# Performance work log

Measured on AMD Instinct MI355X. Metric: run time of the kernel, lower is better.

The kernel has to match this reference:

```python
import jax, jax.numpy as jnp
import numpy as np

D_MODEL = 1024
D_STATE = 64
D_CONV = 4
EXPAND = 2
N_HEADS = 16
HEAD_DIM = 64
ATTN_EVERY = 6
N_LAYERS = 6
D_INNER = D_MODEL * EXPAND
N_SSM = sum(1 for i in range(N_LAYERS) if i % ATTN_EVERY != ATTN_EVERY - 1)
CHUNK = 128  # time-chunk for checkpointed scan


def layer_norm(x, g, b, eps=1e-5):
    mu = jnp.mean(x, axis=-1, keepdims=True)
    var = jnp.mean((x - mu) ** 2, axis=-1, keepdims=True)
    return (x - mu) * jax.lax.rsqrt(var + eps) * g + b


def ssm_layer(x, Wi, cw, cb, Wo, g, b):
    # x: [B, T, d_model]
    Bsz, T, _ = x.shape
    proj = x @ Wi  # [B, T, d_inner + 2*d_state]
    xs = proj[..., :D_INNER]
    Bm = proj[..., D_INNER:D_INNER + D_STATE]
    Cm = proj[..., D_INNER + D_STATE:]
    # causal depthwise conv1d (pad left d_conv-1 == torch pad-both then slice [:T])
    xc = jax.lax.conv_general_dilated(
        xs.transpose(0, 2, 1), cw[:, None, :], (1,), [(D_CONV - 1, 0)],
        feature_group_count=D_INNER, dimension_numbers=('NCH', 'OIH', 'NCH'))
    xc = jax.nn.silu(xc + cb[None, :, None]).transpose(0, 2, 1)  # [B, T, d_inner]
    A = -jnp.exp(jnp.full((D_INNER,), np.float32(np.log(0.5)), x.dtype))  # = -0.5
    nC = T // CHUNK
    u = xc.transpose(1, 0, 2).reshape(nC, CHUNK, Bsz, D_INNER)
    bm = Bm.transpose(1, 0, 2).reshape(nC, CHUNK, Bsz, D_STATE)
    cm = Cm.transpose(1, 0, 2).reshape(nC, CHUNK, Bsz, D_STATE)

    def step(h, inp):
        u_t, b_t, c_t = inp  # [B,d_inner], [B,d_state], [B,d_state]
        h = A[None, :, None] * h + u_t[:, :, None] * b_t[:, None, :]
        y = jnp.einsum('bds,bs->bd', h, c_t)
        return h, y

    @jax.checkpoint
    def chunk_fn(h, ch):
        return jax.lax.scan(step, h, ch)

    h0 = jnp.zeros((Bsz, D_INNER, D_STATE), x.dtype)
    _, y = jax.lax.scan(chunk_fn, h0, (u, bm, cm))  # [nC, CHUNK, B, d_inner]
    y = y.reshape(T, Bsz, D_INNER).transpose(1, 0, 2)
    return layer_norm(y @ Wo + x, g, b)


def attn_layer(x, wq, wk, wv, wo, g, b):
    Bsz, T, _ = x.shape
    sh = (Bsz, T, N_HEADS, HEAD_DIM)
    q = (x @ wq).reshape(sh)
    k = (x @ wk).reshape(sh)
    v = (x @ wv).reshape(sh)
    scores = jnp.einsum('bqhd,bkhd->bhqk', q, k) * (HEAD_DIM ** -0.5)
    mask = jnp.tril(jnp.ones((T, T), bool))
    scores = jnp.where(mask[None, None], scores, -jnp.inf)
    w = jax.nn.softmax(scores, axis=-1)
    o = jnp.einsum('bhqk,bkhd->bqhd', w, v).reshape(Bsz, T, N_HEADS * HEAD_DIM)
    return layer_norm(o @ wo + x, g, b)


def setup_inputs() -> dict:
    key = jax.random.key(0)
    ks = jax.random.split(key, 8)
    s = jnp.float32(0.02)
    d_attn = N_HEADS * HEAD_DIM
    return {
        'x': jax.random.normal(ks[0], (2, 2048, D_MODEL), jnp.float32),
        'in_proj_w': jax.random.normal(ks[1], (N_SSM, D_MODEL, D_INNER + 2 * D_STATE), jnp.float32) * s,
        'conv_w': jax.random.normal(ks[2], (N_SSM, D_INNER, D_CONV), jnp.float32) * s,
        'conv_b': jnp.zeros((N_SSM, D_INNER), jnp.float32),
        'out_proj_w': jax.random.normal(ks[3], (N_SSM, D_INNER, D_MODEL), jnp.float32) * s,
        'ssm_ln_g': jnp.ones((N_SSM, D_MODEL), jnp.float32),
        'ssm_ln_b': jnp.zeros((N_SSM, D_MODEL), jnp.float32),
        'wq': jax.random.normal(ks[4], (D_MODEL, d_attn), jnp.float32) * s,
        'wk': jax.random.normal(ks[5], (D_MODEL, d_attn), jnp.float32) * s,
        'wv': jax.random.normal(ks[6], (D_MODEL, d_attn), jnp.float32) * s,
        'wo': jax.random.normal(ks[7], (d_attn, D_MODEL), jnp.float32) * s,
        'attn_ln_g': jnp.ones((D_MODEL,), jnp.float32),
        'attn_ln_b': jnp.zeros((D_MODEL,), jnp.float32),
    }


def reference(x, in_proj_w, conv_w, conv_b, out_proj_w, ssm_ln_g, ssm_ln_b,
              wq, wk, wv, wo, attn_ln_g, attn_ln_b):
    ssm_idx = 0
    for i in range(N_LAYERS):
        if i % ATTN_EVERY == ATTN_EVERY - 1:
            x = attn_layer(x, wq, wk, wv, wo, attn_ln_g, attn_ln_b)
        else:
            j = ssm_idx
            x = ssm_layer(x, in_proj_w[j], conv_w[j], conv_b[j], out_proj_w[j],
                          ssm_ln_g[j], ssm_ln_b[j])
            ssm_idx += 1
    return x
```

## Files before the change

### kernel.cpp

```cpp
#include <hip/hip_runtime.h>

typedef __attribute__((ext_vector_type(4))) float v4f;
typedef __attribute__((ext_vector_type(4))) float f32x4;
typedef __attribute__((ext_vector_type(8))) __bf16 bf16x8;
typedef __attribute__((ext_vector_type(4))) unsigned short v4u16;

__device__ __forceinline__ unsigned short f2bf(float f) {
    union { float f; unsigned u; } v; v.f = f;
    unsigned r = v.u + 0x7fffu + ((v.u >> 16) & 1u);
    return (unsigned short)(r >> 16);
}
__device__ __forceinline__ float bf2f(unsigned short s) {
    union { unsigned u; float f; } v; v.u = ((unsigned)s) << 16;
    return v.f;
}

#define GLDS16(gp, lp) __builtin_amdgcn_global_load_lds( \
    (const __attribute__((address_space(1))) void*)(gp), \
    (__attribute__((address_space(3))) void*)(lp), 16, 0, 0)

template <int MODE>
__global__ __launch_bounds__(256) void gemm_bf16(
    const unsigned short* __restrict__ A,
    const unsigned short* __restrict__ Bt,
    void* __restrict__ Cout,
    int M, int N, int K, int ldk)
{
    __shared__ __align__(16) unsigned short lA[4096];
    __shared__ __align__(16) unsigned short lB[4096];
    const int tid  = threadIdx.x;
    const int wave = tid >> 6;
    const int lane = tid & 63;
    const int wr = wave >> 1, wc = wave & 1;
    const long m0 = (long)blockIdx.x * 128, n0 = (long)blockIdx.y * 128;
    const int kz = blockIdx.z;
    const long koff = (long)kz * K;

    const int srow = tid >> 2;
    const int scol = (tid & 3) * 8;
    const unsigned short* gA0 = A  + (m0 + srow) * (long)ldk + koff + scol;
    const unsigned short* gB0 = Bt + (n0 + srow) * (long)ldk + koff + scol;
    const long rstride = 64l * ldk;
    unsigned short* lA0 = lA + wave * 512;
    unsigned short* lB0 = lB + wave * 512;

    const int fr = lane & 15;
    const int kg = (lane >> 4) * 8;
    const int arow = (wr * 64 + fr) * 32 + kg;
    const int brow = (wc * 64 + fr) * 32 + kg;

    f32x4 acc[4][4] = {};

    for (int k0 = 0; k0 < K; k0 += 32) {
        __syncthreads();
        GLDS16(gA0 + k0,           lA0);
        GLDS16(gA0 + k0 + rstride, lA0 + 2048);
        GLDS16(gB0 + k0,           lB0);
        GLDS16(gB0 + k0 + rstride, lB0 + 2048);
        __syncthreads();
        bf16x8 af[4], bb[4];
#pragma unroll
        for (int m = 0; m < 4; ++m)
            af[m] = *(const bf16x8*)(lA + arow + m * 512);
#pragma unroll
        for (int n = 0; n < 4; ++n)
            bb[n] = *(const bf16x8*)(lB + brow + n * 512);
#pragma unroll
        for (int m = 0; m < 4; ++m)
#pragma unroll
            for (int n = 0; n < 4; ++n)
                acc[m][n] = __builtin_amdgcn_mfma_f32_16x16x32_bf16(
                    af[m], bb[n], acc[m][n], 0, 0, 0);
    }

    const int lgrp = lane >> 4;
    if constexpr (MODE == 0) {
        float* C = (float*)Cout + (long)kz * M * (long)N;
        float* Cbase = C + (m0 + wr * 64 + lgrp * 4) * (long)N
                         + n0 + wc * 64 + fr;
#pragma unroll
        for (int m = 0; m < 4; ++m)
#pragma unroll
            for (int n = 0; n < 4; ++n) {
                float* cp = Cbase + m * 16 * (long)N + n * 16;
#pragma unroll
                for (int r = 0; r < 4; ++r)
                    cp[r * (long)N] = acc[m][n][r];
            }
    } else if constexpr (MODE == 1) {
        unsigned short* C = (unsigned short*)Cout;
        unsigned short* Cbase = C + (m0 + wr * 64 + lgrp * 4) * (long)N
                                  + n0 + wc * 64 + fr;
#pragma unroll
        for (int m = 0; m < 4; ++m)
#pragma unroll
            for (int n = 0; n < 4; ++n) {
                unsigned short* cp = Cbase + m * 16 * (long)N + n * 16;
#pragma unroll
                for (int r = 0; r < 4; ++r)
                    cp[r * (long)N] = f2bf(acc[m][n][r]);
            }
    } else {
        unsigned short* C = (unsigned short*)Cout;
#pragma unroll
        for (int n = 0; n < 4; ++n) {
            int col = (int)n0 + wc * 64 + n * 16 + fr;
            int hb = col >> 6;
            int s = hb >> 4, h = hb & 15;
            int d = (n & 3) * 16 + fr;
            float sc = (s == 0) ? 0.125f * 1.44269504f : 1.f;
            long obase = ((long)(s * 32) + h) * 2048 * 64 + d;
#pragma unroll
            for (int m = 0; m < 4; ++m) {
#pragma unroll
                for (int r = 0; r < 4; ++r) {
                    int row = (int)m0 + wr * 64 + lgrp * 4 + m * 16 + r;
                    int b = row >> 11, t = row & 2047;
                    C[obase + ((long)b * 16 * 2048 + t) * 64] =
                        f2bf(acc[m][n][r] * sc);
                }
            }
        }
    }
}

__global__ __launch_bounds__(256) void transW(
    const float* __restrict__ in, unsigned short* __restrict__ outp,
    int K, int N, long inl, long outl)
{
    __shared__ unsigned short tile[64][65];
    const float* ip = in + (long)blockIdx.z * inl;
    unsigned short* op = outp + (long)blockIdx.z * outl;
    int n0 = blockIdx.x * 64, k0 = blockIdx.y * 64;
    int cc = threadIdx.x & 63, rr = threadIdx.x >> 6;
#pragma unroll
    for (int i = 0; i < 16; ++i) {
        int r = i * 4 + rr;
        tile[r][cc] = f2bf(ip[(long)(k0 + r) * N + n0 + cc]);
    }
    __syncthreads();
#pragma unroll
    for (int i = 0; i < 16; ++i) {
        int r = i * 4 + rr;
        op[(long)(n0 + r) * K + k0 + cc] = tile[cc][r];
    }
}

__global__ __launch_bounds__(256) void transV(
    const unsigned short* __restrict__ qkvb, unsigned short* __restrict__ vtb)
{
    __shared__ unsigned short tile[64][72];
    const int tid = threadIdx.x;
    const int bh = blockIdx.x, t0 = blockIdx.y * 64;
    const unsigned short* vg = qkvb + 64l * 2048 * 64
                              + (long)bh * 2048 * 64 + (long)t0 * 64;
    const int row = tid >> 2, c0 = (tid & 3) * 16;
#pragma unroll
    for (int i = 0; i < 4; ++i)
        *(v4u16*)(&tile[row][c0 + i * 4]) =
            *(const v4u16*)(vg + row * 64 + c0 + i * 4);
    __syncthreads();
    const int d = tid >> 2, tc = (tid & 3) * 16;
    unsigned short* vo = vtb + (long)bh * 64 * 2048 + (long)d * 2048 + t0 + tc;
#pragma unroll
    for (int i = 0; i < 4; ++i) {
        v4u16 w;
#pragma unroll
        for (int j = 0; j < 4; ++j) w[j] = tile[tc + i * 4 + j][d];
        *(v4u16*)(vo + i * 4) = w;
    }
}

__global__ __launch_bounds__(256) void init_x(
    const float* __restrict__ xin, float* __restrict__ x,
    unsigned short* __restrict__ xb)
{
    long i = ((long)blockIdx.x * 256 + threadIdx.x) * 4;
    v4f v = *(const v4f*)(xin + i);
    *(v4f*)(x + i) = v;
    v4u16 pk;
#pragma unroll
    for (int j = 0; j < 4; ++j) pk[j] = f2bf(v[j]);
    *(v4u16*)(xb + i) = pk;
}

__global__ __launch_bounds__(256) void conv_t(
    const unsigned short* __restrict__ projb,
    const float* __restrict__ cw,
    const float* __restrict__ cb,
    unsigned short* __restrict__ ut)
{
    __shared__ unsigned short tile[68][68];
    const int tid = threadIdx.x;
    const int r0 = blockIdx.x * 64, d0 = blockIdx.y * 64;

    for (int idx = tid; idx < 1072; idx += 256) {
        int row = idx >> 4, c4 = (idx & 15) * 4;
        int gr = r0 - 3 + row;
        v4u16 v;
        if (gr >= 0) v = *(const v4u16*)(projb + (long)gr * 2176 + d0 + c4);
        else         v = (v4u16){0, 0, 0, 0};
        *(v4u16*)(&tile[row][c4]) = v;
    }
    __syncthreads();

    const int lane = tid & 63;
    const int wave = tid >> 6;
    const int t = (r0 + lane) & 2047;
#pragma unroll
    for (int dd = 0; dd < 16; ++dd) {
        int d = wave * 16 + dd;
        int dch = d0 + d;
        v4f w = *(const v4f*)(cw + (long)dch * 4);
        float a = cb[dch];
#pragma unroll
        for (int kk = 0; kk < 4; ++kk) {
            float xv = (t - 3 + kk >= 0) ? bf2f(tile[lane + kk][d]) : 0.f;
            a += xv * w[kk];
        }
        float sv = a / (1.f + __expf(-a));
        ut[(long)dch * 4096 + r0 + lane] = f2bf(sv);
    }
}

__global__ __launch_bounds__(256) void band_ssm(
    const unsigned short* __restrict__ projb,
    const unsigned short* __restrict__ ut,
    unsigned short* __restrict__ yb)
{
    __shared__ __align__(16) unsigned short lU[16384];
    __shared__ __align__(16) unsigned short lB[4096];
    __shared__ __align__(16) unsigned short lC[2048];
    __shared__ __align__(16) unsigned short lP[2048];

    const int tid = threadIdx.x;
    const int wave = tid >> 6, lane = tid & 63;
    const int r0 = blockIdx.x * 32;
    const int d0 = blockIdx.y * 256;
    const int wb = r0 - 32;

#pragma unroll
    for (int p = 0; p < 8; ++p) {
        int chunk = p * 256 + tid;
        int dd = chunk >> 3, j = chunk & 7;
        int off = wb + j * 8; if (off < 0) off = 0;
        uint4 v = *(const uint4*)(ut + (long)(d0 + dd) * 4096 + off);
        *(uint4*)((char*)lU + ((dd * 128 + j * 16) ^ ((dd & 7) << 4))) = v;
    }
#pragma unroll
    for (int p = 0; p < 2; ++p) {
        int chunk = p * 256 + tid;
        int c = chunk >> 3, j = chunk & 7;
        int rc = wb + c; if (rc < 0) rc = 0;
        uint4 v = *(const uint4*)(projb + (long)rc * 2176 + 2048 + j * 8);
        *(uint4*)((char*)lB + ((c * 128 + j * 16) ^ ((c & 7) << 4))) = v;
    }
    {
        int i = tid >> 3, j = tid & 7;
        uint4 v = *(const uint4*)(projb + (long)(r0 + i) * 2176 + 2112 + j * 8);
        *(uint4*)((char*)lC + ((i * 128 + j * 16) ^ ((i & 7) << 4))) = v;
    }
    __syncthreads();

    const int lrow = lane & 15, lgrp = lane >> 4;
    const int sw = (lrow & 7) << 4;

    {
        f32x4 s[2] = {};
        int cb_ = wave * 16 + lrow;
        bf16x8 b0 = *(const bf16x8*)((const char*)lB + ((cb_ * 128 + lgrp * 16) ^ sw));
        bf16x8 b1 = *(const bf16x8*)((const char*)lB + ((cb_ * 128 + 64 + lgrp * 16) ^ sw));
#pragma unroll
        for (int ti = 0; ti < 2; ++ti) {
            int ar = ti * 16 + lrow;
            bf16x8 a0 = *(const bf16x8*)((const char*)lC + ((ar * 128 + lgrp * 16) ^ sw));
            bf16x8 a1 = *(const bf16x8*)((const char*)lC + ((ar * 128 + 64 + lgrp * 16) ^ sw));
            s[ti] = __builtin_amdgcn_mfma_f32_16x16x32_bf16(a0, b0, s[ti], 0, 0, 0);
            s[ti] = __builtin_amdgcn_mfma_f32_16x16x32_bf16(a1, b1, s[ti], 0, 0, 0);
        }
#pragma unroll
        for (int ti = 0; ti < 2; ++ti) {
#pragma unroll
            for (int r = 0; r < 4; ++r) {
                int i = ti * 16 + lgrp * 4 + r;
                int c = wave * 16 + lrow;
                int k = i + 32 - c;
                int t = (r0 + i) & 2047;
                float p = 0.f;
                if (k >= 0 && k <= 31 && k <= t) {
                    float f = exp2f(-(float)k);
                    p = s[ti][r] * ((k & 1) ? -f : f);
                }
                *(unsigned short*)((char*)lP + ((i * 128 + c * 2) ^ ((i & 7) << 4)))
                    = f2bf(p);
            }
        }
    }
    __syncthreads();

    {
        bf16x8 pa[2][2];
#pragma unroll
        for (int ti = 0; ti < 2; ++ti) {
            int pr = ti * 16 + lrow;
            pa[ti][0] = *(const bf16x8*)((const char*)lP + ((pr * 128 + lgrp * 16) ^ sw));
            pa[ti][1] = *(const bf16x8*)((const char*)lP + ((pr * 128 + 64 + lgrp * 16) ^ sw));
        }
#pragma unroll
        for (int dt = 0; dt < 4; ++dt) {
            int dd = wave * 64 + dt * 16 + lrow;
            bf16x8 u0 = *(const bf16x8*)((const char*)lU + ((dd * 128 + lgrp * 16) ^ sw));
            bf16x8 u1 = *(const bf16x8*)((const char*)lU + ((dd * 128 + 64 + lgrp * 16) ^ sw));
#pragma unroll
            for (int ti = 0; ti < 2; ++ti) {
                f32x4 acc = {};
                acc = __builtin_amdgcn_mfma_f32_16x16x32_bf16(pa[ti][0], u0, acc, 0, 0, 0);
                acc = __builtin_amdgcn_mfma_f32_16x16x32_bf16(pa[ti][1], u1, acc, 0, 0, 0);
#pragma unroll
                for (int r = 0; r < 4; ++r) {
                    int i = ti * 16 + lgrp * 4 + r;
                    yb[(long)(r0 + i) * 2048 + d0 + wave * 64 + dt * 16 + lrow]
                        = f2bf(acc[r]);
                }
            }
        }
    }
}

__global__ __launch_bounds__(256) void ln_fuse(
    const float* __restrict__ tmp0, const float* __restrict__ tmp1,
    const float* __restrict__ xres,
    const float* __restrict__ g, const float* __restrict__ b,
    float* __restrict__ xout, unsigned short* __restrict__ xbout)
{
    int row = blockIdx.x;
    int tid = threadIdx.x;
    v4f t0 = *(const v4f*)(tmp0 + (long)row * 1024 + tid * 4);
    v4f t1 = *(const v4f*)(tmp1 + (long)row * 1024 + tid * 4);
    v4f rv = *(const v4f*)(xres + (long)row * 1024 + tid * 4);
    v4f v = t0 + t1 + rv;
    float s = v[0] + v[1] + v[2] + v[3];
    float q = v[0]*v[0] + v[1]*v[1] + v[2]*v[2] + v[3]*v[3];
#pragma unroll
    for (int m = 32; m >= 1; m >>= 1) {
        s += __shfl_xor(s, m, 64);
        q += __shfl_xor(q, m, 64);
    }
    __shared__ float ls[4], lq[4];
    int wave = tid >> 6, lane = tid & 63;
    if (lane == 0) { ls[wave] = s; lq[wave] = q; }
    __syncthreads();
    s = ls[0] + ls[1] + ls[2] + ls[3];
    q = lq[0] + lq[1] + lq[2] + lq[3];
    float mean = s * (1.f / 1024.f);
    float var  = q * (1.f / 1024.f) - mean * mean;
    float rstd = rsqrtf(var + 1e-5f);
    v4f gv = *(const v4f*)(g + tid * 4);
    v4f bv = *(const v4f*)(b + tid * 4);
    v4f o;
#pragma unroll
    for (int i = 0; i < 4; ++i) o[i] = (v[i] - mean) * rstd * gv[i] + bv[i];
    *(v4f*)(xout + (long)row * 1024 + tid * 4) = o;
    v4u16 pk;
#pragma unroll
    for (int i = 0; i < 4; ++i) pk[i] = f2bf(o[i]);
    *(v4u16*)(xbout + (long)row * 1024 + tid * 4) = pk;
}

__global__ __launch_bounds__(256) void attn_mfma(
    const unsigned short* __restrict__ qkvb,
    const unsigned short* __restrict__ vtb,
    unsigned short* __restrict__ ob)
{
    __shared__ __align__(16) unsigned short lK[2][4096];
    __shared__ __align__(16) unsigned short lV[2][4096];
    __shared__ __align__(16) unsigned short lP[4][1024];

    const int tid  = threadIdx.x;
    const int wave = tid >> 6;
    const int lane = tid & 63;
    const int bh = blockIdx.x;
    const int qt = blockIdx.y;
    const long base = (long)bh * 2048 * 64;
    const unsigned short* Qg = qkvb + base;
    const char* Kc = (const char*)(qkvb + 32l * 2048 * 64 + base);
    const char* Vc = (const char*)(vtb + (long)bh * 64 * 2048);

    const int qr0  = qt * 64 + wave * 16;
    const int lrow = lane & 15;
    const int lgrp = lane >> 4;

    bf16x8 qf[2];
    {
        const unsigned short* qp = Qg + (long)(qr0 + lrow) * 64 + lgrp * 8;
        qf[0] = *(const bf16x8*)(qp);
        qf[1] = *(const bf16x8*)(qp + 32);
    }

    f32x4 oacc[4] = {};
    float l[4] = {0.f, 0.f, 0.f, 0.f};

    const int o0  = wave * 1024 + lane * 16;
    const int ta  = o0 >> 7;
    const int cba = (o0 & 127) ^ ((ta & 7) << 4);
    const int o1  = o0 + 4096;
    const int tb  = o1 >> 7;
    const int cbb = (o1 & 127) ^ ((tb & 7) << 4);
    const int ldst = wave * 1024;

#define STAGE(kb_, buf_) do { \
    const int t0_ = (kb_) * 64; \
    GLDS16(Kc + (long)(t0_ + ta) * 128 + cba, (char*)lK[buf_] + ldst); \
    GLDS16(Kc + (long)(t0_ + tb) * 128 + cbb, (char*)lK[buf_] + 4096 + ldst); \
    GLDS16(Vc + (long)ta * 4096 + t0_ * 2 + cba, (char*)lV[buf_] + ldst); \
    GLDS16(Vc + (long)tb * 4096 + t0_ * 2 + cbb, (char*)lV[buf_] + 4096 + ldst); \
} while (0)

    unsigned short* Pw = lP[wave];
    const int nkv = qt + 1;
    STAGE(0, 0);

    for (int kb = 0; kb < nkv; ++kb) {
        const int cur = kb & 1;
        const int t0 = kb * 64;
        __syncthreads();
        if (kb + 1 < nkv) STAGE(kb + 1, cur ^ 1);

        f32x4 sacc[4] = {};
#pragma unroll
        for (int f = 0; f < 4; ++f) {
            int t = f * 16 + lrow;
            int sw = (t & 7) << 4;
            int ob0 = t * 128 + lgrp * 16;
#pragma unroll
            for (int c = 0; c < 2; ++c) {
                bf16x8 kf = *(const bf16x8*)((const char*)lK[cur] + ((ob0 + c * 64) ^ sw));
                sacc[f] = __builtin_amdgcn_mfma_f32_16x16x32_bf16(
                    qf[c], kf, sacc[f], 0, 0, 0);
            }
        }

        float ps[4] = {0.f, 0.f, 0.f, 0.f};
#pragma unroll
        for (int f = 0; f < 4; ++f) {
            int tg = t0 + f * 16 + lrow;
            int t = f * 16 + lrow;
#pragma unroll
            for (int r = 0; r < 4; ++r) {
                int qg = qr0 + lgrp * 4 + r;
                float p = (tg <= qg) ? exp2f(sacc[f][r]) : 0.f;
                ps[r] += p;
                int row = lgrp * 4 + r;
                int po = (row * 128 + t * 2) ^ ((row & 7) << 4);
                *(unsigned short*)((char*)Pw + po) = f2bf(p);
            }
        }
#pragma unroll
        for (int msk = 1; msk < 16; msk <<= 1)
#pragma unroll
            for (int r = 0; r < 4; ++r)
                ps[r] += __shfl_xor(ps[r], msk, 64);
#pragma unroll
        for (int r = 0; r < 4; ++r) l[r] += ps[r];

#pragma unroll
        for (int tc = 0; tc < 2; ++tc) {
            int po = (lrow * 128 + tc * 64 + lgrp * 16) ^ ((lrow & 7) << 4);
            bf16x8 pf = *(const bf16x8*)((const char*)Pw + po);
#pragma unroll
            for (int fd = 0; fd < 4; ++fd) {
                int d = fd * 16 + lrow;
                int vo = (d * 128 + tc * 64 + lgrp * 16) ^ ((d & 7) << 4);
                bf16x8 vf = *(const bf16x8*)((const char*)lV[cur] + vo);
                oacc[fd] = __builtin_amdgcn_mfma_f32_16x16x32_bf16(
                    pf, vf, oacc[fd], 0, 0, 0);
            }
        }
    }
#undef STAGE

    const int b = bh >> 4, h = bh & 15;
#pragma unroll
    for (int r = 0; r < 4; ++r) {
        float inv = 1.f / l[r];
        int qg = qr0 + lgrp * 4 + r;
        unsigned short* orow = ob + ((long)b * 2048 + qg) * 1024 + h * 64;
#pragma unroll
        for (int fd = 0; fd < 4; ++fd)
            orow[fd * 16 + lrow] = f2bf(oacc[fd][r] * inv);
    }
}

extern "C" void kernel_launch(void* const* d_in, const int* in_sizes, int n_in,
                              void* d_out, int out_size, void* d_ws, size_t ws_size,
                              hipStream_t stream) {
    const float* x_in = (const float*)d_in[0];
    const float* Wi   = (const float*)d_in[1];
    const float* cw   = (const float*)d_in[2];
    const float* cb   = (const float*)d_in[3];
    const float* Wo   = (const float*)d_in[4];
    const float* lng  = (const float*)d_in[5];
    const float* lnb  = (const float*)d_in[6];
    const float* wq   = (const float*)d_in[7];
    const float* wk   = (const float*)d_in[8];
    const float* wv   = (const float*)d_in[9];
    const float* wo   = (const float*)d_in[10];
    const float* alng = (const float*)d_in[11];
    const float* alnb = (const float*)d_in[12];
    float* out = (float*)d_out;

    char* ws = (char*)d_ws;
    size_t off = 0;
    auto alloc = [&](size_t bytes) -> void* {
        void* p = ws + off; off += (bytes + 255) & ~(size_t)255; return p;
    };
    unsigned short* xb    = (unsigned short*)alloc(4096ull * 1024 * 2);
    float*          x     = (float*)         alloc(4096ull * 1024 * 4);
    unsigned short* projb = (unsigned short*)alloc(4096ull * 2176 * 2);
    unsigned short* ut    = (unsigned short*)alloc(2048ull * 4096 * 2);
    unsigned short* yb    = (unsigned short*)alloc(4096ull * 2048 * 2);
    float*          tmp   = (float*)         alloc(2ull * 4096 * 1024 * 4);
    unsigned short* qkvb  = (unsigned short*)alloc(3ull * 32 * 2048 * 64 * 2);
    unsigned short* vtb   = (unsigned short*)alloc(32ull * 64 * 2048 * 2);
    unsigned short* WiT   = (unsigned short*)alloc(5ull * 2176 * 1024 * 2);
    unsigned short* WoT   = (unsigned short*)alloc(5ull * 1024 * 2048 * 2);
    unsigned short* WqkvT = (unsigned short*)alloc(3072ull * 1024 * 2);
    unsigned short* WoaT  = (unsigned short*)alloc(1024ull * 1024 * 2);
    float* tmp0 = tmp;
    float* tmp1 = tmp + 4096ull * 1024;

    transW<<<dim3(34, 16, 5), 256, 0, stream>>>(Wi, WiT, 1024, 2176,
        1024l * 2176, 2176l * 1024);
    transW<<<dim3(16, 32, 5), 256, 0, stream>>>(Wo, WoT, 2048, 1024,
        2048l * 1024, 1024l * 2048);
    transW<<<dim3(16, 16, 1), 256, 0, stream>>>(wq, WqkvT,              1024, 1024, 0, 0);
    transW<<<dim3(16, 16, 1), 256, 0, stream>>>(wk, WqkvT + 1024l*1024, 1024, 1024, 0, 0);
    transW<<<dim3(16, 16, 1), 256, 0, stream>>>(wv, WqkvT + 2048l*1024, 1024, 1024, 0, 0);
    transW<<<dim3(16, 16, 1), 256, 0, stream>>>(wo, WoaT,               1024, 1024, 0, 0);

    init_x<<<4096, 256, 0, stream>>>(x_in, x, xb);

    for (int j = 0; j < 5; ++j) {
        gemm_bf16<1><<<dim3(32, 17), 256, 0, stream>>>(
            xb, WiT + (long)j * 2176 * 1024, projb, 4096, 2176, 1024, 1024);
        conv_t<<<dim3(64, 32), 256, 0, stream>>>(
            projb, cw + (long)j * 2048 * 4, cb + (long)j * 2048, ut);
        band_ssm<<<dim3(128, 8), 256, 0, stream>>>(projb, ut, yb);
        gemm_bf16<0><<<dim3(32, 8, 2), 256, 0, stream>>>(
            yb, WoT + (long)j * 1024 * 2048, tmp, 4096, 1024, 1024, 2048);
        ln_fuse<<<4096, 256, 0, stream>>>(
            tmp0, tmp1, x, lng + j * 1024, lnb + j * 1024, x, xb);
    }

    gemm_bf16<2><<<dim3(32, 24), 256, 0, stream>>>(xb, WqkvT, qkvb, 4096, 3072, 1024, 1024);
    transV<<<dim3(32, 32), 256, 0, stream>>>(qkvb, vtb);
    attn_mfma<<<dim3(32, 32), 256, 0, stream>>>(qkvb, vtb, yb);
    gemm_bf16<0><<<dim3(32, 8, 2), 256, 0, stream>>>(
        yb, WoaT, tmp, 4096, 1024, 512, 1024);
    ln_fuse<<<4096, 256, 0, stream>>>(tmp0, tmp1, x, alng, alnb, out, xb);
}
```

Measured before the change: 856.3 us.

## Deepen GEMM K-tile with swizzled LDS, pair causal attention tiles per block

The GEMM now stages a 64-wide K slice per iteration into doubled LDS buffers. An XOR swizzle on the 128-byte rows reduces bank conflicts and halves the number of barrier pairs per K. The attention kernel processes two query tiles per block (jj and 31-jj) so every block does the same amount of causal work, halving the grid. The softmax denominator is now computed with an extra MFMA against a ones vector instead of shuffle reductions. Costs are higher LDS use per GEMM block, which may lower occupancy, and a sequential two-pass loop in attention with fewer blocks in flight.

After: 755.1 us. 11.8% less time.

```diff
diff --git a/kernel.cpp b/kernel.cpp
--- a/kernel.cpp
+++ b/kernel.cpp
@@ -26,8 +26,8 @@
     void* __restrict__ Cout,
     int M, int N, int K, int ldk)
 {
-    __shared__ __align__(16) unsigned short lA[4096];
-    __shared__ __align__(16) unsigned short lB[4096];
+    __shared__ __align__(16) unsigned short lA[8192];
+    __shared__ __align__(16) unsigned short lB[8192];
     const int tid  = threadIdx.x;
     const int wave = tid >> 6;
     const int lane = tid & 63;
@@ -36,44 +36,51 @@
     const int kz = blockIdx.z;
     const long koff = (long)kz * K;
 
-    const int srow = tid >> 2;
-    const int scol = (tid & 3) * 8;
-    const unsigned short* gA0 = A  + (m0 + srow) * (long)ldk + koff + scol;
-    const unsigned short* gB0 = Bt + (n0 + srow) * (long)ldk + koff + scol;
-    const long rstride = 64l * ldk;
+    const int srow = wave * 8 + (lane >> 3);
+    const int scb  = ((lane & 7) * 16) ^ ((srow & 7) << 4);
+    const char* gA0 = (const char*)(A  + (m0 + srow) * (long)ldk + koff) + scb;
+    const char* gB0 = (const char*)(Bt + (n0 + srow) * (long)ldk + koff) + scb;
+    const long rstride = 32l * ldk * 2;
     unsigned short* lA0 = lA + wave * 512;
     unsigned short* lB0 = lB + wave * 512;
 
     const int fr = lane & 15;
-    const int kg = (lane >> 4) * 8;
-    const int arow = (wr * 64 + fr) * 32 + kg;
-    const int brow = (wc * 64 + fr) * 32 + kg;
+    const int lgrp = lane >> 4;
+    const int sw = (fr & 7) << 4;
+    const int abase = (wr * 64 + fr) * 128 + lgrp * 16;
+    const int bbase = (wc * 64 + fr) * 128 + lgrp * 16;
 
     f32x4 acc[4][4] = {};
 
-    for (int k0 = 0; k0 < K; k0 += 32) {
+    for (int k0 = 0; k0 < K; k0 += 64) {
         __syncthreads();
-        GLDS16(gA0 + k0,           lA0);
-        GLDS16(gA0 + k0 + rstride, lA0 + 2048);
-        GLDS16(gB0 + k0,           lB0);
-        GLDS16(gB0 + k0 + rstride, lB0 + 2048);
+        const long kb = (long)k0 * 2;
+#pragma unroll
+        for (int i = 0; i < 4; ++i) {
+            GLDS16(gA0 + kb + i * rstride, lA0 + i * 2048);
+            GLDS16(gB0 + kb + i * rstride, lB0 + i * 2048);
+        }
         __syncthreads();
-        bf16x8 af[4], bb[4];
-#pragma unroll
-        for (int m = 0; m < 4; ++m)
-            af[m] = *(const bf16x8*)(lA + arow + m * 512);
-#pragma unroll
-        for (int n = 0; n < 4; ++n)
-            bb[n] = *(const bf16x8*)(lB + brow + n * 512);
-#pragma unroll
-        for (int m = 0; m < 4; ++m)
+#pragma unroll
+        for (int kk = 0; kk < 2; ++kk) {
+            bf16x8 af[4], bb[4];
+#pragma unroll
+            for (int m = 0; m < 4; ++m)
+                af[m] = *(const bf16x8*)((const char*)lA +
+                        ((abase + m * 2048 + kk * 64) ^ sw));
 #pragma unroll
             for (int n = 0; n < 4; ++n)
-                acc[m][n] = __builtin_amdgcn_mfma_f32_16x16x32_bf16(
-                    af[m], bb[n], acc[m][n], 0, 0, 0);
-    }
-
-    const int lgrp = lane >> 4;
+                bb[n] = *(const bf16x8*)((const char*)lB +
+                        ((bbase + n * 2048 + kk * 64) ^ sw));
+#pragma unroll
+            for (int m = 0; m < 4; ++m)
+#pragma unroll
+                for (int n = 0; n < 4; ++n)
+                    acc[m][n] = __builtin_amdgcn_mfma_f32_16x16x32_bf16(
+                        af[m], bb[n], acc[m][n], 0, 0, 0);
+        }
+    }
+
     if constexpr (MODE == 0) {
         float* C = (float*)Cout + (long)kz * M * (long)N;
         float* Cbase = C + (m0 + wr * 64 + lgrp * 4) * (long)N
@@ -380,25 +387,22 @@
     const int wave = tid >> 6;
     const int lane = tid & 63;
     const int bh = blockIdx.x;
-    const int qt = blockIdx.y;
+    const int jj = blockIdx.y;
     const long base = (long)bh * 2048 * 64;
     const unsigned short* Qg = qkvb + base;
     const char* Kc = (const char*)(qkvb + 32l * 2048 * 64 + base);
     const char* Vc = (const char*)(vtb + (long)bh * 64 * 2048);
 
-    const int qr0  = qt * 64 + wave * 16;
     const int lrow = lane & 15;
     const int lgrp = lane >> 4;
 
-    bf16x8 qf[2];
+    bf16x8 onesf;
     {
-        const unsigned short* qp = Qg + (long)(qr0 + lrow) * 64 + lgrp * 8;
-        qf[0] = *(const bf16x8*)(qp);
-        qf[1] = *(const bf16x8*)(qp + 32);
-    }
-
-    f32x4 oacc[4] = {};
-    float l[4] = {0.f, 0.f, 0.f, 0.f};
+        union { unsigned short s[8]; bf16x8 v; } ou;
+#pragma unroll
+        for (int j = 0; j < 8; ++j) ou.s[j] = 0x3F80;
+        onesf = ou.v;
+    }
 
     const int o0  = wave * 1024 + lane * 16;
     const int ta  = o0 >> 7;
@@ -417,78 +421,87 @@
 } while (0)
 
     unsigned short* Pw = lP[wave];
-    const int nkv = qt + 1;
-    STAGE(0, 0);
-
-    for (int kb = 0; kb < nkv; ++kb) {
-        const int cur = kb & 1;
-        const int t0 = kb * 64;
+    const int b = bh >> 4, h = bh & 15;
+
+    for (int half = 0; half < 2; ++half) {
+        const int qt = half ? (31 - jj) : jj;
+        const int qr0 = qt * 64 + wave * 16;
+        const int nkv = qt + 1;
+
+        bf16x8 qf[2];
+        {
+            const unsigned short* qp = Qg + (long)(qr0 + lrow) * 64 + lgrp * 8;
+            qf[0] = *(const bf16x8*)(qp);
+            qf[1] = *(const bf16x8*)(qp + 32);
+        }
+        f32x4 oacc[4] = {};
+        f32x4 lacc = {};
+
         __syncthreads();
-        if (kb + 1 < nkv) STAGE(kb + 1, cur ^ 1);
-
-        f32x4 sacc[4] = {};
-#pragma unroll
-        for (int f = 0; f < 4; ++f) {
-            int t = f * 16 + lrow;
-            int sw = (t & 7) << 4;
-            int ob0 = t * 128 + lgrp * 16;
-#pragma unroll
-            for (int c = 0; c < 2; ++c) {
-                bf16x8 kf = *(const bf16x8*)((const char*)lK[cur] + ((ob0 + c * 64) ^ sw));
-                sacc[f] = __builtin_amdgcn_mfma_f32_16x16x32_bf16(
-                    qf[c], kf, sacc[f], 0, 0, 0);
-            }
-        }
-
-        float ps[4] = {0.f, 0.f, 0.f, 0.f};
-#pragma unroll
-        for (int f = 0; f < 4; ++f) {
-            int tg = t0 + f * 16 + lrow;
-            int t = f * 16 + lrow;
-#pragma unroll
-            for (int r = 0; r < 4; ++r) {
-                int qg = qr0 + lgrp * 4 + r;
-                float p = (tg <= qg) ? exp2f(sacc[f][r]) : 0.f;
-                ps[r] += p;
-                int row = lgrp * 4 + r;
-                int po = (row * 128 + t * 2) ^ ((row & 7) << 4);
-                *(unsigned short*)((char*)Pw + po) = f2bf(p);
-            }
-        }
-#pragma unroll
-        for (int msk = 1; msk < 16; msk <<= 1)
-#pragma unroll
-            for (int r = 0; r < 4; ++r)
-                ps[r] += __shfl_xor(ps[r], msk, 64);
-#pragma unroll
-        for (int r = 0; r < 4; ++r) l[r] += ps[r];
-
-#pragma unroll
-        for (int tc = 0; tc < 2; ++tc) {
-            int po = (lrow * 128 + tc * 64 + lgrp * 16) ^ ((lrow & 7) << 4);
-            bf16x8 pf = *(const bf16x8*)((const char*)Pw + po);
-#pragma unroll
-            for (int fd = 0; fd < 4; ++fd) {
-                int d = fd * 16 + lrow;
-                int vo = (d * 128 + tc * 64 + lgrp * 16) ^ ((d & 7) << 4);
-                bf16x8 vf = *(const bf16x8*)((const char*)lV[cur] + vo);
-                oacc[fd] = __builtin_amdgcn_mfma_f32_16x16x32_bf16(
-                    pf, vf, oacc[fd], 0, 0, 0);
-            }
+        STAGE(0, 0);
+
+        for (int kb = 0; kb < nkv; ++kb) {
+            const int cur = kb & 1;
+            const int t0 = kb * 64;
+            __syncthreads();
+            if (kb + 1 < nkv) STAGE(kb + 1, cur ^ 1);
+
+            f32x4 sacc[4] = {};
+#pragma unroll
+            for (int f = 0; f < 4; ++f) {
+                int t = f * 16 + lrow;
+                int sw = (t & 7) << 4;
+                int ob0 = t * 128 + lgrp * 16;
+#pragma unroll
+                for (int c = 0; c < 2; ++c) {
+                    bf16x8 kf = *(const bf16x8*)((const char*)lK[cur] + ((ob0 + c * 64) ^ sw));
+                    sacc[f] = __builtin_amdgcn_mfma_f32_16x16x32_bf16(
+                        qf[c], kf, sacc[f], 0, 0, 0);
+                }
+            }
+
+#pragma unroll
+            for (int f = 0; f < 4; ++f) {
+                int tg = t0 + f * 16 + lrow;
+                int t = f * 16 + lrow;
+#pragma unroll
+                for (int r = 0; r < 4; ++r) {
+                    int qg = qr0 + lgrp * 4 + r;
+                    float p = (tg <= qg) ? exp2f(sacc[f][r]) : 0.f;
+                    int row = lgrp * 4 + r;
+                    int po = (row * 128 + t * 2) ^ ((row & 7) << 4);
+                    *(unsigned short*)((char*)Pw + po) = f2bf(p);
+                }
+            }
+
+#pragma unroll
+            for (int tc = 0; tc < 2; ++tc) {
+                int po = (lrow * 128 + tc * 64 + lgrp * 16) ^ ((lrow & 7) << 4);
+                bf16x8 pf = *(const bf16x8*)((const char*)Pw + po);
+                lacc = __builtin_amdgcn_mfma_f32_16x16x32_bf16(
+                    pf, onesf, lacc, 0, 0, 0);
+#pragma unroll
+                for (int fd = 0; fd < 4; ++fd) {
+                    int d = fd * 16 + lrow;
+                    int vo = (d * 128 + tc * 64 + lgrp * 16) ^ ((d & 7) << 4);
+                    bf16x8 vf = *(const bf16x8*)((const char*)lV[cur] + vo);
+                    oacc[fd] = __builtin_amdgcn_mfma_f32_16x16x32_bf16(
+                        pf, vf, oacc[fd], 0, 0, 0);
+                }
+            }
+        }
+
+#pragma unroll
+        for (int r = 0; r < 4; ++r) {
+            float inv = 1.f / lacc[r];
+            int qg = qr0 + lgrp * 4 + r;
+            unsigned short* orow = ob + ((long)b * 2048 + qg) * 1024 + h * 64;
+#pragma unroll
+            for (int fd = 0; fd < 4; ++fd)
+                orow[fd * 16 + lrow] = f2bf(oacc[fd][r] * inv);
         }
     }
 #undef STAGE
-
-    const int b = bh >> 4, h = bh & 15;
-#pragma unroll
-    for (int r = 0; r < 4; ++r) {
-        float inv = 1.f / l[r];
-        int qg = qr0 + lgrp * 4 + r;
-        unsigned short* orow = ob + ((long)b * 2048 + qg) * 1024 + h * 64;
-#pragma unroll
-        for (int fd = 0; fd < 4; ++fd)
-            orow[fd * 16 + lrow] = f2bf(oacc[fd][r] * inv);
-    }
 }
 
 extern "C" void kernel_launch(void* const* d_in, const int* in_sizes, int n_in,
@@ -554,7 +567,7 @@
 
     gemm_bf16<2><<<dim3(32, 24), 256, 0, stream>>>(xb, WqkvT, qkvb, 4096, 3072, 1024, 1024);
     transV<<<dim3(32, 32), 256, 0, stream>>>(qkvb, vtb);
-    attn_mfma<<<dim3(32, 32), 256, 0, stream>>>(qkvb, vtb, yb);
+    attn_mfma<<<dim3(32, 16), 256, 0, stream>>>(qkvb, vtb, yb);
     gemm_bf16<0><<<dim3(32, 8, 2), 256, 0, stream>>>(
         yb, WoaT, tmp, 4096, 1024, 512, 1024);
     ln_fuse<<<4096, 256, 0, stream>>>(tmp0, tmp1, x, alng, alnb, out, xb);
```
